# Performance work log

Measured on AMD Instinct MI355X. Metric: run time of the kernel, lower is better.

The kernel has to match this reference:

```python
import jax, jax.numpy as jnp
import numpy as np

N_HEADS = 16
KV_HEADS = 4
D_HEAD = 64
D_MODEL = 1024
NUM_BUCKETS = 32
MAX_DISTANCE = 128


def _relative_position_bucket(relative_position, num_buckets=NUM_BUCKETS, max_distance=MAX_DISTANCE):
    # Bidirectional (encoder) T5 bucket function.
    nb = num_buckets // 2
    rel_buckets = (relative_position > 0).astype(jnp.int32) * nb
    rp = jnp.abs(relative_position)
    max_exact = nb // 2
    is_small = rp < max_exact
    rp_safe = jnp.maximum(rp, 1).astype(jnp.float32)
    rp_large = max_exact + (
        jnp.log(rp_safe / max_exact) / np.log(max_distance / max_exact) * (nb - max_exact)
    ).astype(jnp.int32)
    rp_large = jnp.minimum(rp_large, nb - 1)
    return rel_buckets + jnp.where(is_small, rp, rp_large)


def compute_bias(rel_bias, q_len, k_len):
    context_pos = jnp.arange(q_len)[:, None]
    memory_pos = jnp.arange(k_len)[None, :]
    buckets = _relative_position_bucket(memory_pos - context_pos)  # [q, k]
    values = rel_bias[buckets]                                     # [q, k, H]
    return jnp.transpose(values, (2, 0, 1))[None]                  # [1, H, q, k]


def setup_inputs() -> dict:
    key = jax.random.key(0)
    ks = jax.random.split(key, 6)
    scale = D_MODEL ** -0.5
    return {
        "hidden_states": jax.random.normal(ks[0], (4, 2048, D_MODEL), jnp.float32),
        "Wq": jax.random.normal(ks[1], (N_HEADS * D_HEAD, D_MODEL), jnp.float32) * scale,
        "Wk": jax.random.normal(ks[2], (N_HEADS * D_HEAD, D_MODEL), jnp.float32) * scale,
        "Wv": jax.random.normal(ks[3], (N_HEADS * D_HEAD, D_MODEL), jnp.float32) * scale,
        "Wo": jax.random.normal(ks[4], (D_MODEL, N_HEADS * D_HEAD), jnp.float32) * scale,
        "rel_bias": jax.random.normal(ks[5], (NUM_BUCKETS, N_HEADS), jnp.float32),
    }


def reference(hidden_states, Wq, Wk, Wv, Wo, rel_bias):
    B, N, _ = hidden_states.shape
    G = N_HEADS // KV_HEADS
    # projections: torch Linear -> x @ W.T; shape to [b, heads, n, d]
    q = (hidden_states @ Wq.T).reshape(B, N, N_HEADS, D_HEAD).transpose(0, 2, 1, 3)
    k = (hidden_states @ Wk.T).reshape(B, N, N_HEADS, D_HEAD).transpose(0, 2, 1, 3)
    v = (hidden_states @ Wv.T).reshape(B, N, N_HEADS, D_HEAD).transpose(0, 2, 1, 3)
    # split heads into (g, h) groups with h = kv_heads as inner index
    gq = q.reshape(B, G, KV_HEADS, N, D_HEAD)
    gk = k.reshape(B, G, KV_HEADS, N, D_HEAD).mean(axis=1)  # [b, h, n, d]
    gv = v.reshape(B, G, KV_HEADS, N, D_HEAD).mean(axis=1)
    # NOTE: einsum sums queries over the group axis g (faithful to source)
    scores = jnp.einsum('bghnd,bhsd->bhns', gq, gk)
    bias = compute_bias(rel_bias, N, N)                      # [1, H, n, n]
    gbias = bias.reshape(1, G, KV_HEADS, N, N).mean(axis=1)  # [1, h, n, n]
    scores = scores + gbias
    attn = jax.nn.softmax(scores.astype(jnp.float32), axis=-1).astype(scores.dtype)
    out = jnp.einsum('bhns,bhsd->bhnd', attn, gv)
    out = out.transpose(0, 2, 1, 3).reshape(B, N, KV_HEADS * D_HEAD)
    out = jnp.tile(out, (1, 1, G))  # repeat 'b s d -> b s (g d)'
    return out @ Wo.T
```

## Files before the change

kernel.cpp:

```cpp
#include <hip/hip_runtime.h>
#include <math.h>

typedef _Float16 half_t;
typedef _Float16 half4 __attribute__((ext_vector_type(4)));
typedef _Float16 half8 __attribute__((ext_vector_type(8)));
typedef float f32x4 __attribute__((ext_vector_type(4)));

#define LOG2E 1.44269504088896f

__device__ __forceinline__ void gload16(const void* g, void* l) {
    __builtin_amdgcn_global_load_lds(
        (const __attribute__((address_space(1))) unsigned int*)g,
        (__attribute__((address_space(3))) unsigned int*)l, 16, 0, 0);
}

__global__ void prep(const float* __restrict__ Wq, const float* __restrict__ Wk,
                     const float* __restrict__ Wv, const float* __restrict__ Wo,
                     const float* __restrict__ rb,
                     half_t* __restrict__ Wqkv, half_t* __restrict__ Wo_e,
                     float* __restrict__ btab) {
    int idx = blockIdx.x * 256 + threadIdx.x;
    if (idx < 768 * 1024) {
        int row = idx >> 10, col = idx & 1023;
        int sec = row >> 8;
        int r = row & 255;
        int h = r >> 6, d = r & 63;
        const float* W = (sec == 0) ? Wq : ((sec == 1) ? Wk : Wv);
        float s = 0.f;
        #pragma unroll
        for (int g = 0; g < 4; ++g) s += W[((g * 4 + h) * 64 + d) * 1024 + col];
        s *= (sec == 0) ? LOG2E : 0.25f;
        Wqkv[idx] = (half_t)s;
    }
    if (idx < 1024 * 256) {
        int m = idx >> 8, c = idx & 255;
        float s = 0.f;
        #pragma unroll
        for (int g = 0; g < 4; ++g) s += Wo[m * 1024 + g * 256 + c];
        Wo_e[idx] = (half_t)s;
    }
    if (idx < 4 * 4096) {
        int h = idx >> 12, dpos = idx & 4095;
        int delta = dpos - 2048;
        int bucket = (delta > 0) ? 16 : 0;
        int ad = delta < 0 ? -delta : delta;
        if (ad < 8) bucket += ad;
        else {
            int large = 8 + (int)(logf((float)ad * 0.125f) / logf(16.0f) * 8.0f);
            bucket += (large < 15) ? large : 15;
        }
        float s = 0.f;
        #pragma unroll
        for (int g = 0; g < 4; ++g) s += rb[bucket * 16 + g * 4 + h];
        btab[idx] = s * 0.25f * LOG2E;
    }
}

__global__ __launch_bounds__(256) void cvt_hs(const float* __restrict__ hs,
                                              half_t* __restrict__ hsh) {
    int i = (blockIdx.x * 256 + threadIdx.x) * 8;
    f32x4 a = *(const f32x4*)&hs[i];
    f32x4 b = *(const f32x4*)&hs[i + 4];
    half8 o;
    #pragma unroll
    for (int j = 0; j < 4; ++j) { o[j] = (half_t)a[j]; o[4 + j] = (half_t)b[j]; }
    *(half8*)&hsh[i] = o;
}

__global__ __launch_bounds__(256) void gemm_nt_mfma(const half_t* __restrict__ A,
                                                    const half_t* __restrict__ B,
                                                    void* __restrict__ Cptr,
                                                    int M, int N, int K, int store_half) {
    __shared__ __attribute__((aligned(16))) half_t As[128 * 32];
    __shared__ __attribute__((aligned(16))) half_t Bs[64 * 32];
    int tid = threadIdx.x;
    int w = tid >> 6, lane = tid & 63;
    int c = lane & 15, quad = lane >> 4;
    int rowBase = blockIdx.y * 128, colBase = blockIdx.x * 64;
    int wr = (w & 1) * 64, wc = (w >> 1) * 32;

    f32x4 acc[4][2];
    #pragma unroll
    for (int i = 0; i < 4; ++i)
        #pragma unroll
        for (int j = 0; j < 2; ++j) acc[i][j] = (f32x4)(0.f);

    int srow = tid >> 2;
    int kcs = ((tid & 3) ^ (srow & 3)) * 8;
    int xk = (quad ^ (c & 3)) * 8;

    for (int k0 = 0; k0 < K; k0 += 32) {
        __syncthreads();
        gload16(&A[(size_t)(rowBase + srow) * K + k0 + kcs],      &As[w * 512]);
        gload16(&A[(size_t)(rowBase + srow + 64) * K + k0 + kcs], &As[2048 + w * 512]);
        gload16(&B[(size_t)(colBase + srow) * K + k0 + kcs],      &Bs[w * 512]);
        __syncthreads();

        half8 af[4], bf[2];
        #pragma unroll
        for (int i = 0; i < 4; ++i)
            af[i] = *(const half8*)&As[(wr + i * 16 + c) * 32 + xk];
        #pragma unroll
        for (int j = 0; j < 2; ++j)
            bf[j] = *(const half8*)&Bs[(wc + j * 16 + c) * 32 + xk];
        #pragma unroll
        for (int i = 0; i < 4; ++i)
            #pragma unroll
            for (int j = 0; j < 2; ++j)
                acc[i][j] = __builtin_amdgcn_mfma_f32_16x16x32_f16(af[i], bf[j], acc[i][j], 0, 0, 0);
    }

    #pragma unroll
    for (int i = 0; i < 4; ++i)
        #pragma unroll
        for (int j = 0; j < 2; ++j)
            #pragma unroll
            for (int reg = 0; reg < 4; ++reg) {
                size_t row = rowBase + wr + i * 16 + quad * 4 + reg;
                size_t col = colBase + wc + j * 16 + c;
                if (store_half) ((half_t*)Cptr)[row * N + col] = (half_t)acc[i][j][reg];
                else            ((float*)Cptr)[row * N + col] = acc[i][j][reg];
            }
}

__global__ __launch_bounds__(256) void transpose_v(const half_t* __restrict__ qkv,
                                                   half_t* __restrict__ vt) {
    __shared__ __attribute__((aligned(16))) half_t T[64 * 65];
    int tid = threadIdx.x;
    int bh = blockIdx.y;
    int b = bh >> 2, h = bh & 3;
    int n0 = blockIdx.x * 64;

    int n = tid >> 2;
    int dc = (tid & 3) * 16;
    const half_t* src = qkv + (size_t)(b * 2048 + n0 + n) * 768 + 512 + h * 64 + dc;
    half8 v0 = *(const half8*)(src);
    half8 v1 = *(const half8*)(src + 8);
    #pragma unroll
    for (int j = 0; j < 8; ++j) {
        T[(dc + j) * 65 + n] = v0[j];
        T[(dc + 8 + j) * 65 + n] = v1[j];
    }
    __syncthreads();

    int d = tid >> 2;
    int nc = (tid & 3) * 16;
    half8 o0, o1;
    #pragma unroll
    for (int j = 0; j < 8; ++j) {
        o0[j] = T[d * 65 + nc + j];
        o1[j] = T[d * 65 + nc + 8 + j];
    }
    half_t* dst = vt + (size_t)(bh * 64 + d) * 2048 + n0 + nc;
    *(half8*)(dst) = o0;
    *(half8*)(dst + 8) = o1;
}

__global__ __launch_bounds__(256) void attn(const half_t* __restrict__ qkv,
                                            const half_t* __restrict__ vt,
                                            const float* __restrict__ btab,
                                            half_t* __restrict__ Opart,
                                            float* __restrict__ ml) {
    __shared__ __attribute__((aligned(16))) half_t Ks[64 * 64];
    __shared__ __attribute__((aligned(16))) half_t Vts[64 * 64];
    __shared__ __attribute__((aligned(16))) half_t Ps[4 * 16 * 72];
    __shared__ float bstat[1152];

    int tid = threadIdx.x;
    int w = tid >> 6, lane = tid & 63;
    int c = lane & 15, quad = lane >> 4;
    int qt = blockIdx.x, h = blockIdx.y;
    int b = blockIdx.z >> 1, s = blockIdx.z & 1;
    int q0 = qt * 64;
    int bh = b * 4 + h;
    int k0g = s * 1024;

    const half_t* qrow = qkv + (size_t)(b * 2048 + q0 + w * 16 + c) * 768 + h * 64;
    half8 qf0 = *(const half8*)(qrow + quad * 8);
    half8 qf1 = *(const half8*)(qrow + 32 + quad * 8);

    float cpos = btab[h * 4096 + 4095];
    float cneg = btab[h * 4096];

    int bbase = k0g - q0 - 63 + 2048;
    for (int j = tid; j < 1152; j += 256) {
        int gi = bbase + j;
        gi = gi < 0 ? 0 : (gi > 4095 ? 4095 : gi);
        bstat[j] = btab[h * 4096 + gi];
    }

    int srow = tid >> 3;
    int kcs = ((tid & 7) ^ (srow & 7)) * 8;
    const half_t* gK = qkv + (size_t)(b * 2048 + k0g + srow) * 768 + 256 + h * 64 + kcs;
    const half_t* gV = vt + (size_t)(bh * 64 + srow) * 2048 + k0g + kcs;

    f32x4 O[4];
    #pragma unroll
    for (int i = 0; i < 4; ++i) O[i] = (f32x4)(0.f);
    float mrow = -1e30f, lrow = 0.f;

    int rx = c & 7;
    half_t* pw = &Ps[w * 16 * 72];

    for (int it = 0; it < 16; ++it) {
        int ktg = k0g + it * 64;
        __syncthreads();
        {
            const half_t* gKt = gK + (size_t)(it * 64) * 768;
            const half_t* gVt = gV + it * 64;
            gload16(gKt,                     &Ks[w * 512]);
            gload16(gKt + (size_t)32 * 768,  &Ks[2048 + w * 512]);
            gload16(gVt,                     &Vts[w * 512]);
            gload16(gVt + 32 * 2048,         &Vts[2048 + w * 512]);
        }
        __syncthreads();

        f32x4 ST[4];
        #pragma unroll
        for (int kb = 0; kb < 4; ++kb) {
            int row = kb * 16 + c;
            half8 kf0 = *(const half8*)&Ks[row * 64 + (quad ^ rx) * 8];
            half8 kf1 = *(const half8*)&Ks[row * 64 + ((quad + 4) ^ rx) * 8];
            f32x4 a = (f32x4)(0.f);
            a = __builtin_amdgcn_mfma_f32_16x16x32_f16(kf0, qf0, a, 0, 0, 0);
            a = __builtin_amdgcn_mfma_f32_16x16x32_f16(kf1, qf1, a, 0, 0, 0);
            ST[kb] = a;
        }

        float cb;
        if (ktg >= q0 + 191) {
            cb = cpos;
        } else if (ktg + 191 <= q0) {
            cb = cneg;
        } else {
            cb = 0.f;
            int jb = it * 64 + 63 - (w * 16 + c);
            #pragma unroll
            for (int kb = 0; kb < 4; ++kb)
                #pragma unroll
                for (int rg = 0; rg < 4; ++rg)
                    ST[kb][rg] += bstat[jb + kb * 16 + quad * 4 + rg];
        }

        float tmax = -1e30f;
        #pragma unroll
        for (int kb = 0; kb < 4; ++kb)
            #pragma unroll
            for (int rg = 0; rg < 4; ++rg) tmax = fmaxf(tmax, ST[kb][rg]);
        tmax += cb;
        tmax = fmaxf(tmax, __shfl_xor(tmax, 16));
        tmax = fmaxf(tmax, __shfl_xor(tmax, 32));

        float mnew = fmaxf(mrow, tmax);
        float alpha = exp2f(mrow - mnew);
        mrow = mnew;
        float madj = mnew - cb;

        float lsum = 0.f;
        #pragma unroll
        for (int kb = 0; kb < 4; ++kb) {
            half4 pk;
            #pragma unroll
            for (int rg = 0; rg < 4; ++rg) {
                float p = exp2f(ST[kb][rg] - madj);
                lsum += p;
                pk[rg] = (half_t)p;
            }
            *(half4*)&pw[c * 72 + kb * 16 + quad * 4] = pk;
        }
        lsum += __shfl_xor(lsum, 16);
        lsum += __shfl_xor(lsum, 32);
        lrow = lrow * alpha + lsum;

        __asm__ __volatile__("s_waitcnt lgkmcnt(0)" ::: "memory");

        half8 pf0 = *(const half8*)&pw[c * 72 + quad * 8];
        half8 pf1 = *(const half8*)&pw[c * 72 + 32 + quad * 8];
        float alphar[4];
        #pragma unroll
        for (int rg = 0; rg < 4; ++rg) alphar[rg] = __shfl(alpha, quad * 4 + rg);
        #pragma unroll
        for (int db = 0; db < 4; ++db) {
            int row = db * 16 + c;
            f32x4 o = O[db];
            #pragma unroll
            for (int rg = 0; rg < 4; ++rg) o[rg] *= alphar[rg];
            half8 v0 = *(const half8*)&Vts[row * 64 + (quad ^ rx) * 8];
            half8 v1 = *(const half8*)&Vts[row * 64 + ((quad + 4) ^ rx) * 8];
            o = __builtin_amdgcn_mfma_f32_16x16x32_f16(pf0, v0, o, 0, 0, 0);
            o = __builtin_amdgcn_mfma_f32_16x16x32_f16(pf1, v1, o, 0, 0, 0);
            O[db] = o;
        }
    }

    int pb = (bh * 32 + qt) * 2 + s;
    #pragma unroll
    for (int db = 0; db < 4; ++db)
        #pragma unroll
        for (int rg = 0; rg < 4; ++rg)
            Opart[((size_t)pb * 64 + w * 16 + quad * 4 + rg) * 64 + db * 16 + c] =
                (half_t)O[db][rg];
    if (quad == 0) {
        ml[pb * 128 + w * 16 + c] = mrow;
        ml[pb * 128 + 64 + w * 16 + c] = lrow;
    }
}

__global__ __launch_bounds__(256) void merge(const half_t* __restrict__ Opart,
                                             const float* __restrict__ ml,
                                             half_t* __restrict__ ab) {
    int bq = blockIdx.x;
    int bh = bq >> 5, qt = bq & 31;
    int b = bh >> 2, h = bh & 3;
    int row = threadIdx.x >> 2;
    int cg = (threadIdx.x & 3) * 16;
    int p0 = bq * 2, p1 = p0 + 1;
    float m1 = ml[p0 * 128 + row], l1 = ml[p0 * 128 + 64 + row];
    float m2 = ml[p1 * 128 + row], l2 = ml[p1 * 128 + 64 + row];
    float m = fmaxf(m1, m2);
    float w1 = exp2f(m1 - m), w2 = exp2f(m2 - m);
    float inv = 1.f / (l1 * w1 + l2 * w2);
    const half8* o1 = (const half8*)&Opart[((size_t)p0 * 64 + row) * 64 + cg];
    const half8* o2 = (const half8*)&Opart[((size_t)p1 * 64 + row) * 64 + cg];
    half_t* dst = ab + (size_t)(b * 2048 + qt * 64 + row) * 256 + h * 64 + cg;
    #pragma unroll
    for (int v = 0; v < 2; ++v) {
        half8 x = o1[v], y = o2[v], o;
        #pragma unroll
        for (int j = 0; j < 8; ++j)
            o[j] = (half_t)(((float)x[j] * w1 + (float)y[j] * w2) * inv);
        *(half8*)(dst + v * 8) = o;
    }
}

extern "C" void kernel_launch(void* const* d_in, const int* in_sizes, int n_in,
                              void* d_out, int out_size, void* d_ws, size_t ws_size,
                              hipStream_t stream) {
    (void)in_sizes; (void)n_in; (void)out_size; (void)ws_size;
    const float* hs = (const float*)d_in[0];
    const float* Wq = (const float*)d_in[1];
    const float* Wk = (const float*)d_in[2];
    const float* Wv = (const float*)d_in[3];
    const float* Wo = (const float*)d_in[4];
    const float* rb = (const float*)d_in[5];

    char* p = (char*)d_ws;
    half_t* Wqkv = (half_t*)p;            p += 768 * 1024 * 2;
    half_t* Wo_e = (half_t*)p;            p += 1024 * 256 * 2;
    float*  btab = (float*)p;             p += 4 * 4096 * 4;
    char*   hshp = p;                     p += (size_t)8192 * 1024 * 2;
    half_t* qkv  = (half_t*)p;            p += (size_t)8192 * 768 * 2;
    half_t* vt   = (half_t*)p;            p += (size_t)16 * 64 * 2048 * 2;
    half_t* hsh   = (half_t*)hshp;
    half_t* Opart = (half_t*)hshp;
    float*  mlbuf = (float*)(hshp + (size_t)1024 * 64 * 64 * 2);
    half_t* ab    = (half_t*)(hshp + (size_t)9 * 1024 * 1024);
    float*  out  = (float*)d_out;

    prep<<<3072, 256, 0, stream>>>(Wq, Wk, Wv, Wo, rb, Wqkv, Wo_e, btab);
    cvt_hs<<<4096, 256, 0, stream>>>(hs, hsh);

    gemm_nt_mfma<<<dim3(12, 64), 256, 0, stream>>>(hsh, Wqkv, qkv, 8192, 768, 1024, 1);

    transpose_v<<<dim3(32, 16), 256, 0, stream>>>(qkv, vt);

    attn<<<dim3(32, 4, 8), 256, 0, stream>>>(qkv, vt, btab, Opart, mlbuf);
    merge<<<512, 256, 0, stream>>>(Opart, mlbuf, ab);

    gemm_nt_mfma<<<dim3(16, 64), 256, 0, stream>>>(ab, Wo_e, out, 8192, 1024, 256, 0);
}
```

Baseline: 193.5 us.

## Fuse V transpose into QKV GEMM, double-buffer K, read V from global in attention

The QKV GEMM now uses a K-step of 64 with larger LDS tiles, and for V columns it writes transposed V directly, which removes the separate transpose kernel. The attention kernel double-buffers K tiles in LDS with prefetch. It also reads V fragments straight from global memory and swaps the MFMA operand order so the output is transposed, which lets alpha be applied per lane without shuffles. The P buffer gets an XOR swizzle instead of padding, and output stores are vectorized. The risk is that uncached global V loads inside the inner loop add latency, and the larger GEMM tiles reduce occupancy.

Result: slower. 228.6 us (+18.1%).

```diff
diff --git a/kernel.cpp b/kernel.cpp
--- a/kernel.cpp
+++ b/kernel.cpp
@@ -70,9 +70,10 @@
 __global__ __launch_bounds__(256) void gemm_nt_mfma(const half_t* __restrict__ A,
                                                     const half_t* __restrict__ B,
                                                     void* __restrict__ Cptr,
-                                                    int M, int N, int K, int store_half) {
-    __shared__ __attribute__((aligned(16))) half_t As[128 * 32];
-    __shared__ __attribute__((aligned(16))) half_t Bs[64 * 32];
+                                                    int M, int N, int K, int store_half,
+                                                    half_t* __restrict__ vtp) {
+    __shared__ __attribute__((aligned(16))) half_t As[128 * 64];
+    __shared__ __attribute__((aligned(16))) half_t Bs[64 * 64];
     int tid = threadIdx.x;
     int w = tid >> 6, lane = tid & 63;
     int c = lane & 15, quad = lane >> 4;
@@ -85,29 +86,55 @@
         #pragma unroll
         for (int j = 0; j < 2; ++j) acc[i][j] = (f32x4)(0.f);
 
-    int srow = tid >> 2;
-    int kcs = ((tid & 3) ^ (srow & 3)) * 8;
-    int xk = (quad ^ (c & 3)) * 8;
-
-    for (int k0 = 0; k0 < K; k0 += 32) {
+    int srow = tid >> 3;
+    int kcs = ((tid & 7) ^ (srow & 7)) * 8;
+    int rx = c & 7;
+
+    for (int k0 = 0; k0 < K; k0 += 64) {
         __syncthreads();
-        gload16(&A[(size_t)(rowBase + srow) * K + k0 + kcs],      &As[w * 512]);
-        gload16(&A[(size_t)(rowBase + srow + 64) * K + k0 + kcs], &As[2048 + w * 512]);
-        gload16(&B[(size_t)(colBase + srow) * K + k0 + kcs],      &Bs[w * 512]);
+        #pragma unroll
+        for (int p = 0; p < 4; ++p)
+            gload16(&A[(size_t)(rowBase + srow + 32 * p) * K + k0 + kcs],
+                    &As[p * 2048 + w * 512]);
+        #pragma unroll
+        for (int p = 0; p < 2; ++p)
+            gload16(&B[(size_t)(colBase + srow + 32 * p) * K + k0 + kcs],
+                    &Bs[p * 2048 + w * 512]);
         __syncthreads();
 
-        half8 af[4], bf[2];
+        #pragma unroll
+        for (int kh = 0; kh < 2; ++kh) {
+            int xk = ((quad + 4 * kh) ^ rx) * 8;
+            half8 af[4], bf[2];
+            #pragma unroll
+            for (int i = 0; i < 4; ++i)
+                af[i] = *(const half8*)&As[(wr + i * 16 + c) * 64 + xk];
+            #pragma unroll
+            for (int j = 0; j < 2; ++j)
+                bf[j] = *(const half8*)&Bs[(wc + j * 16 + c) * 64 + xk];
+            #pragma unroll
+            for (int i = 0; i < 4; ++i)
+                #pragma unroll
+                for (int j = 0; j < 2; ++j)
+                    acc[i][j] = __builtin_amdgcn_mfma_f32_16x16x32_f16(af[i], bf[j], acc[i][j], 0, 0, 0);
+        }
+    }
+
+    if (vtp && colBase >= 512) {
+        int h = (colBase - 512) >> 6;
         #pragma unroll
         for (int i = 0; i < 4; ++i)
-            af[i] = *(const half8*)&As[(wr + i * 16 + c) * 32 + xk];
-        #pragma unroll
-        for (int j = 0; j < 2; ++j)
-            bf[j] = *(const half8*)&Bs[(wc + j * 16 + c) * 32 + xk];
-        #pragma unroll
-        for (int i = 0; i < 4; ++i)
-            #pragma unroll
-            for (int j = 0; j < 2; ++j)
-                acc[i][j] = __builtin_amdgcn_mfma_f32_16x16x32_f16(af[i], bf[j], acc[i][j], 0, 0, 0);
+            #pragma unroll
+            for (int j = 0; j < 2; ++j) {
+                int row0 = rowBase + wr + i * 16 + quad * 4;
+                int dd = wc + j * 16 + c;
+                int b = row0 >> 11, n = row0 & 2047;
+                half4 pk;
+                #pragma unroll
+                for (int reg = 0; reg < 4; ++reg) pk[reg] = (half_t)acc[i][j][reg];
+                *(half4*)&vtp[((size_t)((b * 4 + h) * 64 + dd)) * 2048 + n] = pk;
+            }
+        return;
     }
 
     #pragma unroll
@@ -123,47 +150,13 @@
             }
 }
 
-__global__ __launch_bounds__(256) void transpose_v(const half_t* __restrict__ qkv,
-                                                   half_t* __restrict__ vt) {
-    __shared__ __attribute__((aligned(16))) half_t T[64 * 65];
-    int tid = threadIdx.x;
-    int bh = blockIdx.y;
-    int b = bh >> 2, h = bh & 3;
-    int n0 = blockIdx.x * 64;
-
-    int n = tid >> 2;
-    int dc = (tid & 3) * 16;
-    const half_t* src = qkv + (size_t)(b * 2048 + n0 + n) * 768 + 512 + h * 64 + dc;
-    half8 v0 = *(const half8*)(src);
-    half8 v1 = *(const half8*)(src + 8);
-    #pragma unroll
-    for (int j = 0; j < 8; ++j) {
-        T[(dc + j) * 65 + n] = v0[j];
-        T[(dc + 8 + j) * 65 + n] = v1[j];
-    }
-    __syncthreads();
-
-    int d = tid >> 2;
-    int nc = (tid & 3) * 16;
-    half8 o0, o1;
-    #pragma unroll
-    for (int j = 0; j < 8; ++j) {
-        o0[j] = T[d * 65 + nc + j];
-        o1[j] = T[d * 65 + nc + 8 + j];
-    }
-    half_t* dst = vt + (size_t)(bh * 64 + d) * 2048 + n0 + nc;
-    *(half8*)(dst) = o0;
-    *(half8*)(dst + 8) = o1;
-}
-
 __global__ __launch_bounds__(256) void attn(const half_t* __restrict__ qkv,
                                             const half_t* __restrict__ vt,
                                             const float* __restrict__ btab,
                                             half_t* __restrict__ Opart,
                                             float* __restrict__ ml) {
-    __shared__ __attribute__((aligned(16))) half_t Ks[64 * 64];
-    __shared__ __attribute__((aligned(16))) half_t Vts[64 * 64];
-    __shared__ __attribute__((aligned(16))) half_t Ps[4 * 16 * 72];
+    __shared__ __attribute__((aligned(16))) half_t Ks[2][64 * 64];
+    __shared__ __attribute__((aligned(16))) half_t Ps[4 * 16 * 64];
     __shared__ float bstat[1152];
 
     int tid = threadIdx.x;
@@ -192,7 +185,11 @@
     int srow = tid >> 3;
     int kcs = ((tid & 7) ^ (srow & 7)) * 8;
     const half_t* gK = qkv + (size_t)(b * 2048 + k0g + srow) * 768 + 256 + h * 64 + kcs;
-    const half_t* gV = vt + (size_t)(bh * 64 + srow) * 2048 + k0g + kcs;
+    const half_t* gVbase = vt + (size_t)(bh * 64) * 2048 + k0g;
+
+    gload16(gK,                    &Ks[0][w * 512]);
+    gload16(gK + (size_t)32 * 768, &Ks[0][2048 + w * 512]);
+    __syncthreads();
 
     f32x4 O[4];
     #pragma unroll
@@ -200,27 +197,26 @@
     float mrow = -1e30f, lrow = 0.f;
 
     int rx = c & 7;
-    half_t* pw = &Ps[w * 16 * 72];
+    half_t* pw = &Ps[w * 16 * 64];
+    int pq0 = (quad >> 1);
+    int pq1 = (quad & 1) * 4;
 
     for (int it = 0; it < 16; ++it) {
+        int cur = it & 1;
+        if (it + 1 < 16) {
+            const half_t* gKn = gK + (size_t)((it + 1) * 64) * 768;
+            gload16(gKn,                    &Ks[cur ^ 1][w * 512]);
+            gload16(gKn + (size_t)32 * 768, &Ks[cur ^ 1][2048 + w * 512]);
+        }
         int ktg = k0g + it * 64;
-        __syncthreads();
-        {
-            const half_t* gKt = gK + (size_t)(it * 64) * 768;
-            const half_t* gVt = gV + it * 64;
-            gload16(gKt,                     &Ks[w * 512]);
-            gload16(gKt + (size_t)32 * 768,  &Ks[2048 + w * 512]);
-            gload16(gVt,                     &Vts[w * 512]);
-            gload16(gVt + 32 * 2048,         &Vts[2048 + w * 512]);
-        }
-        __syncthreads();
+        const half_t* KsC = Ks[cur];
 
         f32x4 ST[4];
         #pragma unroll
         for (int kb = 0; kb < 4; ++kb) {
             int row = kb * 16 + c;
-            half8 kf0 = *(const half8*)&Ks[row * 64 + (quad ^ rx) * 8];
-            half8 kf1 = *(const half8*)&Ks[row * 64 + ((quad + 4) ^ rx) * 8];
+            half8 kf0 = *(const half8*)&KsC[row * 64 + (quad ^ rx) * 8];
+            half8 kf1 = *(const half8*)&KsC[row * 64 + ((quad + 4) ^ rx) * 8];
             f32x4 a = (f32x4)(0.f);
             a = __builtin_amdgcn_mfma_f32_16x16x32_f16(kf0, qf0, a, 0, 0, 0);
             a = __builtin_amdgcn_mfma_f32_16x16x32_f16(kf1, qf1, a, 0, 0, 0);
@@ -266,7 +262,8 @@
                 lsum += p;
                 pk[rg] = (half_t)p;
             }
-            *(half4*)&pw[c * 72 + kb * 16 + quad * 4] = pk;
+            int swch = (kb * 2 + pq0) ^ rx;
+            *(half4*)&pw[c * 64 + swch * 8 + pq1] = pk;
         }
         lsum += __shfl_xor(lsum, 16);
         lsum += __shfl_xor(lsum, 32);
@@ -274,32 +271,32 @@
 
         __asm__ __volatile__("s_waitcnt lgkmcnt(0)" ::: "memory");
 
-        half8 pf0 = *(const half8*)&pw[c * 72 + quad * 8];
-        half8 pf1 = *(const half8*)&pw[c * 72 + 32 + quad * 8];
-        float alphar[4];
-        #pragma unroll
-        for (int rg = 0; rg < 4; ++rg) alphar[rg] = __shfl(alpha, quad * 4 + rg);
+        half8 pf0 = *(const half8*)&pw[c * 64 + (quad ^ rx) * 8];
+        half8 pf1 = *(const half8*)&pw[c * 64 + ((quad + 4) ^ rx) * 8];
         #pragma unroll
         for (int db = 0; db < 4; ++db) {
-            int row = db * 16 + c;
+            const half_t* gV = gVbase + (size_t)(db * 16 + c) * 2048 + it * 64;
+            half8 vf0 = *(const half8*)(gV + quad * 8);
+            half8 vf1 = *(const half8*)(gV + 32 + quad * 8);
             f32x4 o = O[db];
             #pragma unroll
-            for (int rg = 0; rg < 4; ++rg) o[rg] *= alphar[rg];
-            half8 v0 = *(const half8*)&Vts[row * 64 + (quad ^ rx) * 8];
-            half8 v1 = *(const half8*)&Vts[row * 64 + ((quad + 4) ^ rx) * 8];
-            o = __builtin_amdgcn_mfma_f32_16x16x32_f16(pf0, v0, o, 0, 0, 0);
-            o = __builtin_amdgcn_mfma_f32_16x16x32_f16(pf1, v1, o, 0, 0, 0);
+            for (int rg = 0; rg < 4; ++rg) o[rg] *= alpha;
+            o = __builtin_amdgcn_mfma_f32_16x16x32_f16(vf0, pf0, o, 0, 0, 0);
+            o = __builtin_amdgcn_mfma_f32_16x16x32_f16(vf1, pf1, o, 0, 0, 0);
             O[db] = o;
         }
+
+        __syncthreads();
     }
 
     int pb = (bh * 32 + qt) * 2 + s;
     #pragma unroll
-    for (int db = 0; db < 4; ++db)
-        #pragma unroll
-        for (int rg = 0; rg < 4; ++rg)
-            Opart[((size_t)pb * 64 + w * 16 + quad * 4 + rg) * 64 + db * 16 + c] =
-                (half_t)O[db][rg];
+    for (int db = 0; db < 4; ++db) {
+        half4 pk;
+        #pragma unroll
+        for (int rg = 0; rg < 4; ++rg) pk[rg] = (half_t)O[db][rg];
+        *(half4*)&Opart[((size_t)pb * 64 + w * 16 + c) * 64 + db * 16 + quad * 4] = pk;
+    }
     if (quad == 0) {
         ml[pb * 128 + w * 16 + c] = mrow;
         ml[pb * 128 + 64 + w * 16 + c] = lrow;
@@ -360,12 +357,10 @@
     prep<<<3072, 256, 0, stream>>>(Wq, Wk, Wv, Wo, rb, Wqkv, Wo_e, btab);
     cvt_hs<<<4096, 256, 0, stream>>>(hs, hsh);
 
-    gemm_nt_mfma<<<dim3(12, 64), 256, 0, stream>>>(hsh, Wqkv, qkv, 8192, 768, 1024, 1);
-
-    transpose_v<<<dim3(32, 16), 256, 0, stream>>>(qkv, vt);
+    gemm_nt_mfma<<<dim3(12, 64), 256, 0, stream>>>(hsh, Wqkv, qkv, 8192, 768, 1024, 1, vt);
 
     attn<<<dim3(32, 4, 8), 256, 0, stream>>>(qkv, vt, btab, Opart, mlbuf);
     merge<<<512, 256, 0, stream>>>(Opart, mlbuf, ab);
 
-    gemm_nt_mfma<<<dim3(16, 64), 256, 0, stream>>>(ab, Wo_e, out, 8192, 1024, 256, 0);
-}
+    gemm_nt_mfma<<<dim3(16, 64), 256, 0, stream>>>(ab, Wo_e, out, 8192, 1024, 256, 0, nullptr);
+}
```
